# Kernel optimization log

Measured on AMD Instinct MI355X. Metric: run time of the kernel, lower is better.

Reference implementation:

```python
import jax, jax.numpy as jnp
import numpy as np

EMB_DIM = 1024
NHEAD = 16
HEAD_DIM = EMB_DIM // NHEAD
SLEN = 1024
BSZ = 8
NEG_INF = -1e30


def setup_inputs() -> dict:
    key = jax.random.key(0)
    ks = jax.random.split(key, 8)
    q = jax.random.normal(ks[0], (SLEN, BSZ, EMB_DIM), dtype=jnp.float32)
    k = jax.random.normal(ks[1], (SLEN, BSZ, EMB_DIM), dtype=jnp.float32)
    v = jax.random.normal(ks[2], (SLEN, BSZ, EMB_DIM), dtype=jnp.float32)
    mask = jax.random.randint(ks[3], (BSZ * NHEAD, SLEN, SLEN), 0, 2).astype(jnp.bool_)
    # xavier_uniform bound for square [E,E] matrices
    bound = float(np.sqrt(6.0 / (EMB_DIM + EMB_DIM)))
    Wq = jax.random.uniform(ks[4], (EMB_DIM, EMB_DIM), jnp.float32, -bound, bound)
    Wk = jax.random.uniform(ks[5], (EMB_DIM, EMB_DIM), jnp.float32, -bound, bound)
    Wv = jax.random.uniform(ks[6], (EMB_DIM, EMB_DIM), jnp.float32, -bound, bound)
    Wo = jax.random.uniform(ks[7], (EMB_DIM, EMB_DIM), jnp.float32, -bound, bound)
    return {"q": q, "k": k, "v": v, "mask": mask, "Wq": Wq, "Wk": Wk, "Wv": Wv, "Wo": Wo}


def reference(q, k, v, mask, Wq, Wk, Wv, Wo):
    slen, bsz, emb = q.shape
    scaling = float(HEAD_DIM) ** -0.5
    # F.linear(x, W) = x @ W.T
    query = q @ Wq.T  # [slen, bsz, E]
    key_ = k @ Wk.T
    value = v @ Wv.T
    # -> [bsz*nhead, slen, head_dim]
    def split_heads(x):
        return x.reshape(slen, bsz * NHEAD, HEAD_DIM).transpose(1, 0, 2)
    query = split_heads(query)
    key_ = split_heads(key_)
    value = split_heads(value)
    attn_weight = jnp.einsum('bqd,bkd->bqk', query, key_) * scaling  # [B*H, S, S]
    attn_weight = jnp.where(mask, NEG_INF, attn_weight)
    attn_score = jax.nn.softmax(attn_weight, axis=-1)
    # attn_mask=True: post-softmax multiplicative mask
    attn_score = attn_score * (~mask).astype(attn_score.dtype)
    # dropout is identity in eval mode
    attn_output = jnp.einsum('bqk,bkd->bqd', attn_score, value)  # [B*H, S, hd]
    attn_output = attn_output.transpose(1, 0, 2).reshape(slen, bsz, emb)
    return attn_output @ Wo.T
```

## Files before the change

### kernel.cpp

```cpp
#include <hip/hip_runtime.h>


typedef __attribute__((ext_vector_type(8))) short bf16x8;
typedef __attribute__((ext_vector_type(8))) unsigned short u16x8;
typedef __attribute__((ext_vector_type(4))) float f32x4;

#define LOG2E 1.44269504088896340736f

__device__ __forceinline__ unsigned short bfbits(float f) {
  unsigned u = __builtin_bit_cast(unsigned, f);
  u += 0x7fffu + ((u >> 16) & 1u);
  return (unsigned short)(u >> 16);
}
__device__ __forceinline__ unsigned pk2(float a, float b) {
  return (unsigned)bfbits(a) | ((unsigned)bfbits(b) << 16);
}
__device__ __forceinline__ void async16(const void* src, void* dst_lds) {
  __builtin_amdgcn_global_load_lds(
      (const __attribute__((address_space(1))) unsigned int*)src,
      (__attribute__((address_space(3))) unsigned int*)dst_lds, 16, 0, 0);
}

__global__ __launch_bounds__(256) void cvt_kernel(
    const float* __restrict__ q, const float* __restrict__ k, const float* __restrict__ v,
    const float* __restrict__ wq, const float* __restrict__ wk,
    const float* __restrict__ wv, const float* __restrict__ wo,
    unsigned short* __restrict__ Xin, unsigned short* __restrict__ Wbf)
{
  const unsigned u = blockIdx.x * 256u + threadIdx.x;
  const float* src;
  unsigned short* dst;
  if (u < 3145728u) {
    const unsigned z = u >> 20, r = u & 1048575u;
    src = (z == 0 ? q : z == 1 ? k : v) + (size_t)r * 8;
    dst = Xin + (size_t)z * 8388608u + (size_t)r * 8;
  } else {
    const unsigned u2 = u - 3145728u, wz = u2 >> 17, r = u2 & 131071u;
    src = (wz == 0 ? wq : wz == 1 ? wk : wz == 2 ? wv : wo) + (size_t)r * 8;
    dst = Wbf + (size_t)wz * 1048576u + (size_t)r * 8;
  }
  f32x4 a = *(const f32x4*)src;
  f32x4 b = *(const f32x4*)(src + 4);
  u16x8 o;
  o[0]=bfbits(a[0]); o[1]=bfbits(a[1]); o[2]=bfbits(a[2]); o[3]=bfbits(a[3]);
  o[4]=bfbits(b[0]); o[5]=bfbits(b[1]); o[6]=bfbits(b[2]); o[7]=bfbits(b[3]);
  *(u16x8*)dst = o;
}

__global__ void detect_mask(const unsigned* __restrict__ m, int* __restrict__ flag)
{
  unsigned ok = 1u;
#pragma unroll 8
  for (int i = 0; i < 64; ++i) {
    unsigned w = m[(threadIdx.x << 6) + i];
    ok &= (w <= 1u) ? 1u : 0u;
  }
  unsigned long long vote = __ballot(ok != 0u);
  if (threadIdx.x == 0) *flag = (vote == ~0ull) ? 1 : 0;
}

template<int OUTF32>
__global__ __launch_bounds__(512) void gemm2ph(
    const unsigned short* __restrict__ A,
    const unsigned short* __restrict__ B,
    void* __restrict__ Cv, float scale, int M, int N, int K)
{
  const int tid = threadIdx.x;
  const int w = tid >> 6, lane = tid & 63, c = lane & 15, g = lane >> 4;
  const int wr = w >> 1, wc = w & 1;

  const int nwg = gridDim.x, cpx = nwg >> 3, bid = blockIdx.x;
  const int swz = (bid & 7) * cpx + (bid >> 3);
  const int ntx = N >> 7;
  const int bx = swz % ntx, by = swz / ntx;
  const int rowA = by * 256, rowB = bx * 128;

  __shared__ unsigned short As[2][256 * 64];
  __shared__ unsigned short Bs[2][128 * 64];

  f32x4 acc[4][4];
#pragma unroll
  for (int i = 0; i < 4; ++i)
#pragma unroll
    for (int j = 0; j < 4; ++j) acc[i][j] = (f32x4){0.f, 0.f, 0.f, 0.f};

  const int srow = tid >> 3, skc = tid & 7;
  const int wbase = (tid & ~63) * 16;

#pragma unroll
  for (int i = 0; i < 4; ++i)
    async16(A + (size_t)(rowA + i * 64 + srow) * K + skc * 8,
            (char*)&As[0][0] + i * 8192 + wbase);
#pragma unroll
  for (int j = 0; j < 2; ++j)
    async16(B + (size_t)(rowB + j * 64 + srow) * K + skc * 8,
            (char*)&Bs[0][0] + j * 8192 + wbase);
  __syncthreads();

  int buf = 0;
  const int nk = K >> 6;
  for (int kt = 0; kt < nk; ++kt) {
    if (kt + 1 < nk) {
      const int k1 = (kt + 1) << 6, bo = buf ^ 1;
#pragma unroll
      for (int i = 0; i < 4; ++i)
        async16(A + (size_t)(rowA + i * 64 + srow) * K + k1 + skc * 8,
                (char*)&As[bo][0] + i * 8192 + wbase);
#pragma unroll
      for (int j = 0; j < 2; ++j)
        async16(B + (size_t)(rowB + j * 64 + srow) * K + k1 + skc * 8,
                (char*)&Bs[bo][0] + j * 8192 + wbase);
    }
    bf16x8 af[4][2], bfr[4][2];
#pragma unroll
    for (int x = 0; x < 4; ++x)
#pragma unroll
      for (int ks = 0; ks < 2; ++ks) {
        af[x][ks]  = *(const bf16x8*)&As[buf][(wr * 64 + x * 16 + c) * 64 + ks * 32 + (g << 3)];
        bfr[x][ks] = *(const bf16x8*)&Bs[buf][(wc * 64 + x * 16 + c) * 64 + ks * 32 + (g << 3)];
      }
#pragma unroll
    for (int ks = 0; ks < 2; ++ks)
#pragma unroll
      for (int mf = 0; mf < 4; ++mf)
#pragma unroll
        for (int nf = 0; nf < 4; ++nf)
          acc[mf][nf] = __builtin_amdgcn_mfma_f32_16x16x32_bf16(af[mf][ks], bfr[nf][ks], acc[mf][nf], 0, 0, 0);
    __syncthreads();
    buf ^= 1;
  }

  const int r0 = rowA + wr * 64, c0 = rowB + wc * 64;
  if (OUTF32) {
    float* O = (float*)Cv;
#pragma unroll
    for (int mf = 0; mf < 4; ++mf)
#pragma unroll
      for (int nf = 0; nf < 4; ++nf)
#pragma unroll
        for (int j = 0; j < 4; ++j)
          O[(size_t)(r0 + mf * 16 + g * 4 + j) * N + c0 + nf * 16 + c] = acc[mf][nf][j] * scale;
  } else {
    unsigned short* O = (unsigned short*)Cv;
#pragma unroll
    for (int mf = 0; mf < 4; ++mf)
#pragma unroll
      for (int nf = 0; nf < 4; ++nf)
#pragma unroll
        for (int j = 0; j < 4; ++j)
          O[(size_t)(r0 + mf * 16 + g * 4 + j) * N + c0 + nf * 16 + c] = bfbits(acc[mf][nf][j] * scale);
  }
}

__global__ __launch_bounds__(256) void transpose_v(
    const unsigned short* __restrict__ Xp2, unsigned short* __restrict__ Vt)
{
  const int tid = threadIdx.x;
  const int bh = blockIdx.y, b = bh >> 4, h = bh & 15;
  const int s0 = blockIdx.x << 6;
  __shared__ unsigned short T[64 * 68];
#pragma unroll
  for (int p = 0; p < 2; ++p) {
    const int idx = (p << 8) + tid, sr = idx >> 3, ch2 = idx & 7;
    *(u16x8*)&T[sr * 68 + ch2 * 8] =
        *(const u16x8*)(Xp2 + ((size_t)((s0 + sr) * 8 + b) << 10) + (h << 6) + ch2 * 8);
  }
  __syncthreads();
#pragma unroll
  for (int p = 0; p < 2; ++p) {
    const int idx = (p << 8) + tid, dr = idx >> 3, ch2 = idx & 7;
    u16x8 o;
#pragma unroll
    for (int e = 0; e < 8; ++e) o[e] = T[(ch2 * 8 + e) * 68 + dr];
    *(u16x8*)(Vt + ((size_t)(bh * 64 + dr) << 10) + s0 + ch2 * 8) = o;
  }
}

__device__ __forceinline__ void load_mask4(unsigned mv[4], const void* maskp, bool mi32,
                                           size_t base, int g) {
  if (mi32) {
    const int* mrow = (const int*)maskp + base + (g << 2);
#pragma unroll
    for (int mf = 0; mf < 4; ++mf) {
      const int4 w4 = *(const int4*)(mrow + mf * 16);
      mv[mf] = (w4.x ? 1u : 0u) | (w4.y ? 0x100u : 0u) | (w4.z ? 0x10000u : 0u) | (w4.w ? 0x1000000u : 0u);
    }
  } else {
    const unsigned char* mrow = (const unsigned char*)maskp + base + (g << 2);
#pragma unroll
    for (int mf = 0; mf < 4; ++mf) mv[mf] = *(const unsigned*)(mrow + mf * 16);
  }
}

__global__ __launch_bounds__(256) void attn_kernel(
    const unsigned short* __restrict__ Qp,
    const unsigned short* __restrict__ Kp,
    const unsigned short* __restrict__ Vt,
    const void*           __restrict__ maskp,
    const int*            __restrict__ mflag,
    unsigned short* __restrict__ AO)
{
  const int tid = threadIdx.x;
  const int w = tid >> 6, lane = tid & 63, c = lane & 15, g = lane >> 4;
  const int bh = blockIdx.y, b = bh >> 4, h = bh & 15;
  const int qb0 = blockIdx.x << 6;
  const int qrow = qb0 + (w << 4) + c;
  const bool mi32 = (*mflag != 0);

  __shared__ unsigned short Ksm[64 * 72];
  __shared__ unsigned short Vsm[64 * 72];
  __shared__ unsigned short Psm[4][16 * 72];

  bf16x8 qf[2];
  {
    const unsigned short* qp = Qp + ((size_t)(qrow * 8 + b) << 10) + (h << 6) + (g << 3);
    qf[0] = *(const bf16x8*)qp;
    qf[1] = *(const bf16x8*)(qp + 32);
  }

  const int row0 = tid >> 3, ch = tid & 7;
  const unsigned short* Vg = Vt + ((size_t)bh << 16);
  const size_t mbase0 = ((size_t)bh << 20) + ((size_t)qrow << 10);

  bf16x8 kr[2], vr[2];
#pragma unroll
  for (int p = 0; p < 2; ++p) {
    const int r = row0 + p * 32;
    kr[p] = *(const bf16x8*)(Kp + ((size_t)(r * 8 + b) << 10) + (h << 6) + (ch << 3));
    vr[p] = *(const bf16x8*)(Vg + ((size_t)r << 10) + (ch << 3));
  }
  unsigned mv[4];
  load_mask4(mv, maskp, mi32, mbase0, g);

  f32x4 oacc[4];
#pragma unroll
  for (int i = 0; i < 4; ++i) oacc[i] = (f32x4){0.f, 0.f, 0.f, 0.f};
  float mrun = -1e30f, lrun = 0.f;

  for (int t = 0; t < 16; ++t) {
    const int kk0 = t << 6;
    __syncthreads();
#pragma unroll
    for (int p = 0; p < 2; ++p) {
      const int r = row0 + p * 32;
      *(bf16x8*)&Ksm[r * 72 + (ch << 3)] = kr[p];
      *(bf16x8*)&Vsm[r * 72 + (ch << 3)] = vr[p];
    }
    __syncthreads();
    unsigned mvN[4];
    if (t < 15) {
      const int kk1 = kk0 + 64;
#pragma unroll
      for (int p = 0; p < 2; ++p) {
        const int r = row0 + p * 32;
        kr[p] = *(const bf16x8*)(Kp + ((size_t)((kk1 + r) * 8 + b) << 10) + (h << 6) + (ch << 3));
        vr[p] = *(const bf16x8*)(Vg + ((size_t)r << 10) + kk1 + (ch << 3));
      }
      load_mask4(mvN, maskp, mi32, mbase0 + kk1, g);
    }
    f32x4 sacc[4];
#pragma unroll
    for (int i = 0; i < 4; ++i) sacc[i] = (f32x4){0.f, 0.f, 0.f, 0.f};
#pragma unroll
    for (int d2 = 0; d2 < 2; ++d2) {
#pragma unroll
      for (int mf = 0; mf < 4; ++mf) {
        bf16x8 kf = *(const bf16x8*)&Ksm[(mf * 16 + c) * 72 + d2 * 32 + (g << 3)];
        sacc[mf] = __builtin_amdgcn_mfma_f32_16x16x32_bf16(kf, qf[d2], sacc[mf], 0, 0, 0);
      }
    }
    float tmax = -1e30f;
#pragma unroll
    for (int mf = 0; mf < 4; ++mf)
#pragma unroll
      for (int j = 0; j < 4; ++j) {
        float s = sacc[mf][j];
        if ((mv[mf] >> (8 * j)) & 0xffu) s = -1e30f;
        sacc[mf][j] = s;
        tmax = fmaxf(tmax, s);
      }
    tmax = fmaxf(tmax, __shfl_xor(tmax, 16));
    tmax = fmaxf(tmax, __shfl_xor(tmax, 32));
    const float mnew = fmaxf(mrun, tmax);
    const float alpha = __builtin_amdgcn_exp2f((mrun - mnew) * LOG2E);
    float tsum = 0.f;
    float pv[4][4];
#pragma unroll
    for (int mf = 0; mf < 4; ++mf)
#pragma unroll
      for (int j = 0; j < 4; ++j) {
        const float p = __builtin_amdgcn_exp2f((sacc[mf][j] - mnew) * LOG2E);
        pv[mf][j] = p;
        tsum += p;
      }
    tsum += __shfl_xor(tsum, 16);
    tsum += __shfl_xor(tsum, 32);
    lrun = lrun * alpha + tsum;
    mrun = mnew;
#pragma unroll
    for (int i = 0; i < 4; ++i) {
      oacc[i][0] *= alpha; oacc[i][1] *= alpha; oacc[i][2] *= alpha; oacc[i][3] *= alpha;
    }
#pragma unroll
    for (int mf = 0; mf < 4; ++mf) {
      uint2 t2;
      t2.x = pk2(pv[mf][0], pv[mf][1]);
      t2.y = pk2(pv[mf][2], pv[mf][3]);
      *(uint2*)&Psm[w][c * 72 + mf * 16 + (g << 2)] = t2;
    }
#pragma unroll
    for (int ks = 0; ks < 2; ++ks) {
      bf16x8 pf = *(const bf16x8*)&Psm[w][c * 72 + ks * 32 + (g << 3)];
#pragma unroll
      for (int mf = 0; mf < 4; ++mf) {
        bf16x8 vf = *(const bf16x8*)&Vsm[(mf * 16 + c) * 72 + ks * 32 + (g << 3)];
        oacc[mf] = __builtin_amdgcn_mfma_f32_16x16x32_bf16(vf, pf, oacc[mf], 0, 0, 0);
      }
    }
    if (t < 15) {
      mv[0] = mvN[0]; mv[1] = mvN[1]; mv[2] = mvN[2]; mv[3] = mvN[3];
    }
  }
  const float inv = 1.0f / lrun;
#pragma unroll
  for (int mf = 0; mf < 4; ++mf) {
    uint2 t2;
    t2.x = pk2(oacc[mf][0] * inv, oacc[mf][1] * inv);
    t2.y = pk2(oacc[mf][2] * inv, oacc[mf][3] * inv);
    *(uint2*)(AO + ((size_t)(qrow * 8 + b) << 10) + (h << 6) + mf * 16 + (g << 2)) = t2;
  }
}

extern "C" void kernel_launch(void* const* d_in, const int* in_sizes, int n_in,
                              void* d_out, int out_size, void* d_ws, size_t ws_size,
                              hipStream_t stream)
{
  const float* q  = (const float*)d_in[0];
  const float* k  = (const float*)d_in[1];
  const float* v  = (const float*)d_in[2];
  const void*  mask = (const void*)d_in[3];
  const float* wq = (const float*)d_in[4];
  const float* wk = (const float*)d_in[5];
  const float* wv = (const float*)d_in[6];
  const float* wo = (const float*)d_in[7];

  unsigned short* ws  = (unsigned short*)d_ws;
  unsigned short* Xin = ws;
  unsigned short* Wbf = ws + 25165824u;
  unsigned short* Xp  = ws + 29360128u;
  unsigned short* Vt  = ws + 8388608u;
  unsigned short* AO  = ws;
  int* mfl            = (int*)(ws + 16777216u);

  cvt_kernel<<<14336, 256, 0, stream>>>(q, k, v, wq, wk, wv, wo, Xin, Wbf);
  gemm2ph<0><<<256, 512, 0, stream>>>(Xin,             Wbf,            Xp,             0.125f, 8192, 1024, 1024);
  gemm2ph<0><<<256, 512, 0, stream>>>(Xin + 8388608u,  Wbf + 1048576u, Xp + 8388608u,  1.0f,   8192, 1024, 1024);
  gemm2ph<0><<<256, 512, 0, stream>>>(Xin + 16777216u, Wbf + 2097152u, Xp + 16777216u, 1.0f,   8192, 1024, 1024);
  detect_mask<<<1, 64, 0, stream>>>((const unsigned*)mask, mfl);
  transpose_v<<<dim3(16, 128), 256, 0, stream>>>(Xp + 16777216u, Vt);
  attn_kernel<<<dim3(16, 128), 256, 0, stream>>>(Xp, Xp + 8388608u, Vt, mask, mfl, AO);
  gemm2ph<1><<<256, 512, 0, stream>>>(AO, Wbf + 3145728u, d_out, 1.0f, 8192, 1024, 1024);
}
```

Before: 311.6 us.

## Swizzle GEMM LDS layout, deepen load pipeline, add MFMA priority hints

```diff
diff --git a/kernel.cpp b/kernel.cpp
--- a/kernel.cpp
+++ b/kernel.cpp
@@ -19,6 +19,18 @@
   __builtin_amdgcn_global_load_lds(
       (const __attribute__((address_space(1))) unsigned int*)src,
       (__attribute__((address_space(3))) unsigned int*)dst_lds, 16, 0, 0);
+}
+
+__global__ void detect_mask(const unsigned* __restrict__ m, int* __restrict__ flag)
+{
+  unsigned ok = 1u;
+#pragma unroll 8
+  for (int i = 0; i < 64; ++i) {
+    unsigned w = m[(threadIdx.x << 6) + i];
+    ok &= (w <= 1u) ? 1u : 0u;
+  }
+  unsigned long long vote = __ballot(ok != 0u);
+  if (threadIdx.x == 0) *flag = (vote == ~0ull) ? 1 : 0;
 }
 
 __global__ __launch_bounds__(256) void cvt_kernel(
@@ -41,22 +53,10 @@
   }
   f32x4 a = *(const f32x4*)src;
   f32x4 b = *(const f32x4*)(src + 4);
-  u16x8 o;
-  o[0]=bfbits(a[0]); o[1]=bfbits(a[1]); o[2]=bfbits(a[2]); o[3]=bfbits(a[3]);
-  o[4]=bfbits(b[0]); o[5]=bfbits(b[1]); o[6]=bfbits(b[2]); o[7]=bfbits(b[3]);
-  *(u16x8*)dst = o;
-}
-
-__global__ void detect_mask(const unsigned* __restrict__ m, int* __restrict__ flag)
-{
-  unsigned ok = 1u;
-#pragma unroll 8
-  for (int i = 0; i < 64; ++i) {
-    unsigned w = m[(threadIdx.x << 6) + i];
-    ok &= (w <= 1u) ? 1u : 0u;
-  }
-  unsigned long long vote = __ballot(ok != 0u);
-  if (threadIdx.x == 0) *flag = (vote == ~0ull) ? 1 : 0;
+  uint4 o;
+  o.x = pk2(a[0], a[1]); o.y = pk2(a[2], a[3]);
+  o.z = pk2(b[0], b[1]); o.w = pk2(b[2], b[3]);
+  *(uint4*)dst = o;
 }
 
 template<int OUTF32>
@@ -69,8 +69,8 @@
   const int w = tid >> 6, lane = tid & 63, c = lane & 15, g = lane >> 4;
   const int wr = w >> 1, wc = w & 1;
 
-  const int nwg = gridDim.x, cpx = nwg >> 3, bid = blockIdx.x;
-  const int swz = (bid & 7) * cpx + (bid >> 3);
+  const int bid = blockIdx.x;
+  const int swz = (bid & 7) * 32 + (bid >> 3);
   const int ntx = N >> 7;
   const int bx = swz % ntx, by = swz / ntx;
   const int rowA = by * 256, rowB = bx * 128;
@@ -84,51 +84,58 @@
 #pragma unroll
     for (int j = 0; j < 4; ++j) acc[i][j] = (f32x4){0.f, 0.f, 0.f, 0.f};
 
-  const int srow = tid >> 3, skc = tid & 7;
+  const int srow = tid >> 3;
+  const int skc = (tid & 7) ^ (srow & 7);
   const int wbase = (tid & ~63) * 16;
 
-#pragma unroll
-  for (int i = 0; i < 4; ++i)
-    async16(A + (size_t)(rowA + i * 64 + srow) * K + skc * 8,
-            (char*)&As[0][0] + i * 8192 + wbase);
-#pragma unroll
-  for (int j = 0; j < 2; ++j)
-    async16(B + (size_t)(rowB + j * 64 + srow) * K + skc * 8,
-            (char*)&Bs[0][0] + j * 8192 + wbase);
-  __syncthreads();
-
-  int buf = 0;
-  const int nk = K >> 6;
-  for (int kt = 0; kt < nk; ++kt) {
-    if (kt + 1 < nk) {
-      const int k1 = (kt + 1) << 6, bo = buf ^ 1;
-#pragma unroll
-      for (int i = 0; i < 4; ++i)
-        async16(A + (size_t)(rowA + i * 64 + srow) * K + k1 + skc * 8,
-                (char*)&As[bo][0] + i * 8192 + wbase);
-#pragma unroll
-      for (int j = 0; j < 2; ++j)
-        async16(B + (size_t)(rowB + j * 64 + srow) * K + k1 + skc * 8,
-                (char*)&Bs[bo][0] + j * 8192 + wbase);
-    }
-    bf16x8 af[4][2], bfr[4][2];
-#pragma unroll
-    for (int x = 0; x < 4; ++x)
-#pragma unroll
-      for (int ks = 0; ks < 2; ++ks) {
-        af[x][ks]  = *(const bf16x8*)&As[buf][(wr * 64 + x * 16 + c) * 64 + ks * 32 + (g << 3)];
-        bfr[x][ks] = *(const bf16x8*)&Bs[buf][(wc * 64 + x * 16 + c) * 64 + ks * 32 + (g << 3)];
-      }
-#pragma unroll
-    for (int ks = 0; ks < 2; ++ks)
-#pragma unroll
-      for (int mf = 0; mf < 4; ++mf)
-#pragma unroll
-        for (int nf = 0; nf < 4; ++nf)
-          acc[mf][nf] = __builtin_amdgcn_mfma_f32_16x16x32_bf16(af[mf][ks], bfr[nf][ks], acc[mf][nf], 0, 0, 0);
-    __syncthreads();
-    buf ^= 1;
-  }
+#define STAGE(kt_, bb_) do { const int k0_ = (kt_) << 6;                          \
+    _Pragma("unroll") for (int i_ = 0; i_ < 4; ++i_)                              \
+      async16(A + (size_t)(rowA + i_ * 64 + srow) * K + k0_ + skc * 8,            \
+              (char*)&As[bb_][0] + i_ * 8192 + wbase);                            \
+    _Pragma("unroll") for (int j_ = 0; j_ < 2; ++j_)                              \
+      async16(B + (size_t)(rowB + j_ * 64 + srow) * K + k0_ + skc * 8,            \
+              (char*)&Bs[bb_][0] + j_ * 8192 + wbase); } while (0)
+
+#define RD(arr_, bb_, row_, ks_) \
+    (*(const bf16x8*)&arr_[bb_][(row_) * 64 + ((((ks_) * 4 + g) ^ (c & 7)) << 3)])
+
+#define COMPUTE(bb_) do {                                                         \
+    bf16x8 af_[4][2], bf_[4][2];                                                  \
+    _Pragma("unroll") for (int x_ = 0; x_ < 4; ++x_)                              \
+      _Pragma("unroll") for (int ks_ = 0; ks_ < 2; ++ks_) {                       \
+        af_[x_][ks_] = RD(As, bb_, wr * 64 + x_ * 16 + c, ks_);                   \
+        bf_[x_][ks_] = RD(Bs, bb_, wc * 64 + x_ * 16 + c, ks_);                   \
+      }                                                                           \
+    _Pragma("unroll") for (int ks_ = 0; ks_ < 2; ++ks_)                           \
+      _Pragma("unroll") for (int mf_ = 0; mf_ < 4; ++mf_)                         \
+        _Pragma("unroll") for (int nf_ = 0; nf_ < 4; ++nf_)                       \
+          acc[mf_][nf_] = __builtin_amdgcn_mfma_f32_16x16x32_bf16(                \
+              af_[mf_][ks_], bf_[nf_][ks_], acc[mf_][nf_], 0, 0, 0); } while (0)
+
+  STAGE(0, 0);
+  STAGE(1, 1);
+
+  for (int kt = 0; kt < 15; ++kt) {
+    asm volatile("s_waitcnt vmcnt(6)" ::: "memory");
+    __builtin_amdgcn_sched_barrier(0);
+    __builtin_amdgcn_s_barrier();
+    __builtin_amdgcn_sched_barrier(0);
+    const int buf = kt & 1;
+    COMPUTE(buf);
+    __builtin_amdgcn_sched_barrier(0);
+    __builtin_amdgcn_s_barrier();
+    __builtin_amdgcn_sched_barrier(0);
+    if (kt < 14) STAGE(kt + 2, buf);
+  }
+  asm volatile("s_waitcnt vmcnt(0)" ::: "memory");
+  __builtin_amdgcn_sched_barrier(0);
+  __builtin_amdgcn_s_barrier();
+  __builtin_amdgcn_sched_barrier(0);
+  COMPUTE(1);
+
+#undef STAGE
+#undef RD
+#undef COMPUTE
 
   const int r0 = rowA + wr * 64, c0 = rowB + wc * 64;
   if (OUTF32) {
@@ -261,6 +268,7 @@
     f32x4 sacc[4];
 #pragma unroll
     for (int i = 0; i < 4; ++i) sacc[i] = (f32x4){0.f, 0.f, 0.f, 0.f};
+    __builtin_amdgcn_s_setprio(1);
 #pragma unroll
     for (int d2 = 0; d2 < 2; ++d2) {
 #pragma unroll
@@ -269,6 +277,7 @@
         sacc[mf] = __builtin_amdgcn_mfma_f32_16x16x32_bf16(kf, qf[d2], sacc[mf], 0, 0, 0);
       }
     }
+    __builtin_amdgcn_s_setprio(0);
     float tmax = -1e30f;
 #pragma unroll
     for (int mf = 0; mf < 4; ++mf)
@@ -308,6 +317,7 @@
       t2.y = pk2(pv[mf][2], pv[mf][3]);
       *(uint2*)&Psm[w][c * 72 + mf * 16 + (g << 2)] = t2;
     }
+    __builtin_amdgcn_s_setprio(1);
 #pragma unroll
     for (int ks = 0; ks < 2; ++ks) {
       bf16x8 pf = *(const bf16x8*)&Psm[w][c * 72 + ks * 32 + (g << 3)];
@@ -317,9 +327,9 @@
         oacc[mf] = __builtin_amdgcn_mfma_f32_16x16x32_bf16(vf, pf, oacc[mf], 0, 0, 0);
       }
     }
-    if (t < 15) {
-      mv[0] = mvN[0]; mv[1] = mvN[1]; mv[2] = mvN[2]; mv[3] = mvN[3];
-    }
+    __builtin_amdgcn_s_setprio(0);
+#pragma unroll
+    for (int i = 0; i < 4; ++i) mv[i] = mvN[i];
   }
   const float inv = 1.0f / lrun;
 #pragma unroll
@@ -348,15 +358,15 @@
   unsigned short* Xin = ws;
   unsigned short* Wbf = ws + 25165824u;
   unsigned short* Xp  = ws + 29360128u;
+  int* mfl            = (int*)(ws + 54525952u);
   unsigned short* Vt  = ws + 8388608u;
   unsigned short* AO  = ws;
-  int* mfl            = (int*)(ws + 16777216u);
-
+
+  detect_mask<<<1, 64, 0, stream>>>((const unsigned*)mask, mfl);
   cvt_kernel<<<14336, 256, 0, stream>>>(q, k, v, wq, wk, wv, wo, Xin, Wbf);
   gemm2ph<0><<<256, 512, 0, stream>>>(Xin,             Wbf,            Xp,             0.125f, 8192, 1024, 1024);
   gemm2ph<0><<<256, 512, 0, stream>>>(Xin + 8388608u,  Wbf + 1048576u, Xp + 8388608u,  1.0f,   8192, 1024, 1024);
   gemm2ph<0><<<256, 512, 0, stream>>>(Xin + 16777216u, Wbf + 2097152u, Xp + 16777216u, 1.0f,   8192, 1024, 1024);
-  detect_mask<<<1, 64, 0, stream>>>((const unsigned*)mask, mfl);
   transpose_v<<<dim3(16, 128), 256, 0, stream>>>(Xp + 16777216u, Vt);
   attn_kernel<<<dim3(16, 128), 256, 0, stream>>>(Xp, Xp + 8388608u, Vt, mask, mfl, AO);
   gemm2ph<1><<<256, 512, 0, stream>>>(AO, Wbf + 3145728u, d_out, 1.0f, 8192, 1024, 1024);
```

Result: no change. 309.4 us (-0.7%).
